# Performance work log

Measured on AMD Instinct MI355X. Metric: run time of the kernel, lower is better.

Reference implementation:

```python
import jax, jax.numpy as jnp
import numpy as np

EPS = 1e-05
N_CLUSTERS = 4


def setup_inputs() -> dict:
    key = jax.random.key(0)
    k1, k2, k3, k4, k5, k6 = jax.random.split(key, 6)
    B, C, H, W = 64, 64, 112, 112
    return {
        "x": jax.random.normal(k1, (B, C, H, W), dtype=jnp.float32),
        "running_mean": jax.random.normal(k2, (C,), dtype=jnp.float32),
        "running_var": jax.random.uniform(k3, (C,), dtype=jnp.float32),
        "weight": jax.random.normal(k4, (C,), dtype=jnp.float32),
        "bias": jax.random.normal(k5, (C,), dtype=jnp.float32),
        "labels": jax.random.randint(k6, (B,), 0, N_CLUSTERS, dtype=jnp.int32),
    }


def reference(x, running_mean, running_var, weight, bias, labels):
    B, C, H, W = x.shape
    hw = H * W
    # per-sample partial sums over spatial dims -> [B, C]
    s = jnp.sum(x, axis=(2, 3))
    ss = jnp.sum(x * x, axis=(2, 3))
    # per-cluster reductions over the batch (gather-reduce) -> [G, C]
    S = jax.ops.segment_sum(s, labels, num_segments=N_CLUSTERS)
    SS = jax.ops.segment_sum(ss, labels, num_segments=N_CLUSTERS)
    cnt = jax.ops.segment_sum(jnp.ones((B,), x.dtype), labels, num_segments=N_CLUSTERS)
    N = cnt[:, None] * hw  # elements per (cluster, channel)
    mean_g = S / jnp.maximum(N, 1.0)
    # unbiased variance (ddof=1), matching torch.var_mean(unbiased=True)
    var_g = (SS - N * mean_g * mean_g) / jnp.maximum(N - 1.0, 1.0)
    # blended stats: 0.2 * cluster + 0.8 * running (BN source) stats; scatter back per sample
    mu = 0.2 * mean_g[labels] + 0.8 * running_mean[None, :]      # [B, C]
    var = 0.2 * var_g[labels] + 0.8 * running_var[None, :]       # [B, C]
    x_n = (x - mu[:, :, None, None]) * jax.lax.rsqrt(var + EPS)[:, :, None, None]
    return x_n * weight[None, :, None, None] + bias[None, :, None, None]
```

## Files before the change

kernel.cpp:

```cpp
#include <hip/hip_runtime.h>

#define HW    12544
#define HW4   3136
#define NCH   64
#define NB    64
#define EPSF  1e-5f

typedef float fvec4 __attribute__((ext_vector_type(4)));


__global__ __launch_bounds__(256) void cn_stats_half(const float* __restrict__ x,
                                                     float* __restrict__ ws,
                                                     int c0) {
    int c = (blockIdx.x & 31) + c0;
    int b = blockIdx.x >> 5;
    int p = b * NCH + c;
    const fvec4* xp = (const fvec4*)(x + (size_t)p * HW);
    float s = 0.0f, ss = 0.0f;
    for (int i = threadIdx.x; i < HW4; i += 256) {
        fvec4 v = xp[i];
        s  += v.x + v.y + v.z + v.w;
        ss += v.x * v.x + v.y * v.y + v.z * v.z + v.w * v.w;
    }
    #pragma unroll
    for (int off = 32; off > 0; off >>= 1) {
        s  += __shfl_down(s, off, 64);
        ss += __shfl_down(ss, off, 64);
    }
    __shared__ float sh[8];
    int lane = threadIdx.x & 63;
    int wave = threadIdx.x >> 6;
    if (lane == 0) { sh[wave] = s; sh[4 + wave] = ss; }
    __syncthreads();
    if (threadIdx.x == 0) {
        ws[p]        = sh[0] + sh[1] + sh[2] + sh[3];
        ws[4096 + p] = sh[4] + sh[5] + sh[6] + sh[7];
    }
}

__global__ __launch_bounds__(256) void cn_norm_half(const float* __restrict__ x,
                                                    const int* __restrict__ labels,
                                                    const float* __restrict__ rmean,
                                                    const float* __restrict__ rvar,
                                                    const float* __restrict__ wgt,
                                                    const float* __restrict__ bia,
                                                    const float* __restrict__ ws,
                                                    float* __restrict__ out,
                                                    int c0) {
    int c = (blockIdx.x & 31) + c0;
    int b = blockIdx.x >> 5;
    int p = b * NCH + c;
    __shared__ float sh_scale, sh_shift;
    if (threadIdx.x < 64) {
        int t = threadIdx.x;
        int g  = labels[b];
        int lb = labels[t];
        bool m = (lb == g);
        float s   = m ? ws[t * NCH + c]        : 0.0f;
        float ss  = m ? ws[4096 + t * NCH + c] : 0.0f;
        float cnt = m ? 1.0f : 0.0f;
        #pragma unroll
        for (int off = 32; off > 0; off >>= 1) {
            s   += __shfl_down(s,   off, 64);
            ss  += __shfl_down(ss,  off, 64);
            cnt += __shfl_down(cnt, off, 64);
        }
        if (t == 0) {
            float N    = cnt * (float)HW;
            float mean = s / fmaxf(N, 1.0f);
            float var  = (ss - N * mean * mean) / fmaxf(N - 1.0f, 1.0f);
            float mu   = 0.2f * mean + 0.8f * rmean[c];
            float vb   = 0.2f * var  + 0.8f * rvar[c];
            float scale = rsqrtf(vb + EPSF) * wgt[c];
            sh_scale = scale;
            sh_shift = bia[c] - mu * scale;
        }
    }
    __syncthreads();
    float scale = sh_scale;
    float shift = sh_shift;
    const fvec4* xp = (const fvec4*)(x + (size_t)p * HW);
    fvec4*       op = (fvec4*)(out + (size_t)p * HW);
    for (int i = threadIdx.x; i < HW4; i += 256) {
        fvec4 v = __builtin_nontemporal_load(&xp[i]);
        fvec4 o;
        o.x = v.x * scale + shift;
        o.y = v.y * scale + shift;
        o.z = v.z * scale + shift;
        o.w = v.w * scale + shift;
        __builtin_nontemporal_store(o, &op[i]);
    }
}

extern "C" void kernel_launch(void* const* d_in, const int* in_sizes, int n_in,
                              void* d_out, int out_size, void* d_ws, size_t ws_size,
                              hipStream_t stream) {
    const float* x      = (const float*)d_in[0];
    const float* rmean  = (const float*)d_in[1];
    const float* rvar   = (const float*)d_in[2];
    const float* wgt    = (const float*)d_in[3];
    const float* bia    = (const float*)d_in[4];
    const int*   labels = (const int*)d_in[5];
    float* out = (float*)d_out;
    float* ws  = (float*)d_ws;

    const int half = NB * (NCH / 2);

    cn_stats_half<<<half, 256, 0, stream>>>(x, ws, 0);
    cn_norm_half <<<half, 256, 0, stream>>>(x, labels, rmean, rvar, wgt, bia, ws, out, 0);
    cn_stats_half<<<half, 256, 0, stream>>>(x, ws, 32);
    cn_norm_half <<<half, 256, 0, stream>>>(x, labels, rmean, rvar, wgt, bia, ws, out, 32);
}
```

Baseline: 101.2 us.

## Pipeline channel-chunk stats with normalization of the previous chunk in one launch

Replaces the two-half stats/normalize sequence with nine launches over 8-channel chunks. Each launch computes statistics for chunk k while normalizing chunk k-1, so the second read of x hits a much smaller, more cache-resident working set and the two phases overlap. The normalize path also switches from a nontemporal load to a regular load so it can reuse the cached data. The cost is more kernel launches and a boundary between launches for each chunk.

```diff
diff --git a/kernel.cpp b/kernel.cpp
--- a/kernel.cpp
+++ b/kernel.cpp
@@ -9,86 +9,87 @@
 typedef float fvec4 __attribute__((ext_vector_type(4)));
 
 
-__global__ __launch_bounds__(256) void cn_stats_half(const float* __restrict__ x,
-                                                     float* __restrict__ ws,
-                                                     int c0) {
-    int c = (blockIdx.x & 31) + c0;
-    int b = blockIdx.x >> 5;
-    int p = b * NCH + c;
-    const fvec4* xp = (const fvec4*)(x + (size_t)p * HW);
-    float s = 0.0f, ss = 0.0f;
-    for (int i = threadIdx.x; i < HW4; i += 256) {
-        fvec4 v = xp[i];
-        s  += v.x + v.y + v.z + v.w;
-        ss += v.x * v.x + v.y * v.y + v.z * v.z + v.w * v.w;
-    }
-    #pragma unroll
-    for (int off = 32; off > 0; off >>= 1) {
-        s  += __shfl_down(s, off, 64);
-        ss += __shfl_down(ss, off, 64);
-    }
-    __shared__ float sh[8];
-    int lane = threadIdx.x & 63;
-    int wave = threadIdx.x >> 6;
-    if (lane == 0) { sh[wave] = s; sh[4 + wave] = ss; }
-    __syncthreads();
-    if (threadIdx.x == 0) {
-        ws[p]        = sh[0] + sh[1] + sh[2] + sh[3];
-        ws[4096 + p] = sh[4] + sh[5] + sh[6] + sh[7];
-    }
-}
+__global__ __launch_bounds__(256) void cn_pipe(const float* __restrict__ x,
+                                               const int* __restrict__ labels,
+                                               const float* __restrict__ rmean,
+                                               const float* __restrict__ rvar,
+                                               const float* __restrict__ wgt,
+                                               const float* __restrict__ bia,
+                                               float* __restrict__ ws,
+                                               float* __restrict__ out,
+                                               int c_stats0, int c_norm0) {
+    int half = blockIdx.x >> 9;
+    int idx  = blockIdx.x & 511;
+    int cc   = idx & 7;
+    int b    = idx >> 3;
 
-__global__ __launch_bounds__(256) void cn_norm_half(const float* __restrict__ x,
-                                                    const int* __restrict__ labels,
-                                                    const float* __restrict__ rmean,
-                                                    const float* __restrict__ rvar,
-                                                    const float* __restrict__ wgt,
-                                                    const float* __restrict__ bia,
-                                                    const float* __restrict__ ws,
-                                                    float* __restrict__ out,
-                                                    int c0) {
-    int c = (blockIdx.x & 31) + c0;
-    int b = blockIdx.x >> 5;
-    int p = b * NCH + c;
-    __shared__ float sh_scale, sh_shift;
-    if (threadIdx.x < 64) {
-        int t = threadIdx.x;
-        int g  = labels[b];
-        int lb = labels[t];
-        bool m = (lb == g);
-        float s   = m ? ws[t * NCH + c]        : 0.0f;
-        float ss  = m ? ws[4096 + t * NCH + c] : 0.0f;
-        float cnt = m ? 1.0f : 0.0f;
+    if (half == 1 || c_norm0 < 0) {
+        int c = c_stats0 + cc;
+        int p = b * NCH + c;
+        const fvec4* xp = (const fvec4*)(x + (size_t)p * HW);
+        float s = 0.0f, ss = 0.0f;
+        for (int i = threadIdx.x; i < HW4; i += 256) {
+            fvec4 v = xp[i];
+            s  += v.x + v.y + v.z + v.w;
+            ss += v.x * v.x + v.y * v.y + v.z * v.z + v.w * v.w;
+        }
         #pragma unroll
         for (int off = 32; off > 0; off >>= 1) {
-            s   += __shfl_down(s,   off, 64);
-            ss  += __shfl_down(ss,  off, 64);
-            cnt += __shfl_down(cnt, off, 64);
+            s  += __shfl_down(s, off, 64);
+            ss += __shfl_down(ss, off, 64);
         }
-        if (t == 0) {
-            float N    = cnt * (float)HW;
-            float mean = s / fmaxf(N, 1.0f);
-            float var  = (ss - N * mean * mean) / fmaxf(N - 1.0f, 1.0f);
-            float mu   = 0.2f * mean + 0.8f * rmean[c];
-            float vb   = 0.2f * var  + 0.8f * rvar[c];
-            float scale = rsqrtf(vb + EPSF) * wgt[c];
-            sh_scale = scale;
-            sh_shift = bia[c] - mu * scale;
+        __shared__ float sh[8];
+        int lane = threadIdx.x & 63;
+        int wave = threadIdx.x >> 6;
+        if (lane == 0) { sh[wave] = s; sh[4 + wave] = ss; }
+        __syncthreads();
+        if (threadIdx.x == 0) {
+            ws[p]        = sh[0] + sh[1] + sh[2] + sh[3];
+            ws[4096 + p] = sh[4] + sh[5] + sh[6] + sh[7];
         }
-    }
-    __syncthreads();
-    float scale = sh_scale;
-    float shift = sh_shift;
-    const fvec4* xp = (const fvec4*)(x + (size_t)p * HW);
-    fvec4*       op = (fvec4*)(out + (size_t)p * HW);
-    for (int i = threadIdx.x; i < HW4; i += 256) {
-        fvec4 v = __builtin_nontemporal_load(&xp[i]);
-        fvec4 o;
-        o.x = v.x * scale + shift;
-        o.y = v.y * scale + shift;
-        o.z = v.z * scale + shift;
-        o.w = v.w * scale + shift;
-        __builtin_nontemporal_store(o, &op[i]);
+    } else {
+        int c = c_norm0 + cc;
+        int p = b * NCH + c;
+        __shared__ float sh_scale, sh_shift;
+        if (threadIdx.x < 64) {
+            int t  = threadIdx.x;
+            int g  = labels[b];
+            int lb = labels[t];
+            bool m = (lb == g);
+            float s   = m ? ws[t * NCH + c]        : 0.0f;
+            float ss  = m ? ws[4096 + t * NCH + c] : 0.0f;
+            float cnt = m ? 1.0f : 0.0f;
+            #pragma unroll
+            for (int off = 32; off > 0; off >>= 1) {
+                s   += __shfl_down(s,   off, 64);
+                ss  += __shfl_down(ss,  off, 64);
+                cnt += __shfl_down(cnt, off, 64);
+            }
+            if (t == 0) {
+                float N    = cnt * (float)HW;
+                float mean = s / fmaxf(N, 1.0f);
+                float var  = (ss - N * mean * mean) / fmaxf(N - 1.0f, 1.0f);
+                float mu   = 0.2f * mean + 0.8f * rmean[c];
+                float vb   = 0.2f * var  + 0.8f * rvar[c];
+                float scale = rsqrtf(vb + EPSF) * wgt[c];
+                sh_scale = scale;
+                sh_shift = bia[c] - mu * scale;
+            }
+        }
+        __syncthreads();
+        float scale = sh_scale;
+        float shift = sh_shift;
+        const fvec4* xp = (const fvec4*)(x + (size_t)p * HW);
+        fvec4*       op = (fvec4*)(out + (size_t)p * HW);
+        for (int i = threadIdx.x; i < HW4; i += 256) {
+            fvec4 v = xp[i];
+            fvec4 o;
+            o.x = v.x * scale + shift;
+            o.y = v.y * scale + shift;
+            o.z = v.z * scale + shift;
+            o.w = v.w * scale + shift;
+            __builtin_nontemporal_store(o, &op[i]);
+        }
     }
 }
 
@@ -104,10 +105,10 @@
     float* out = (float*)d_out;
     float* ws  = (float*)d_ws;
 
-    const int half = NB * (NCH / 2);
-
-    cn_stats_half<<<half, 256, 0, stream>>>(x, ws, 0);
-    cn_norm_half <<<half, 256, 0, stream>>>(x, labels, rmean, rvar, wgt, bia, ws, out, 0);
-    cn_stats_half<<<half, 256, 0, stream>>>(x, ws, 32);
-    cn_norm_half <<<half, 256, 0, stream>>>(x, labels, rmean, rvar, wgt, bia, ws, out, 32);
+    cn_pipe<<<512, 256, 0, stream>>>(x, labels, rmean, rvar, wgt, bia, ws, out, 0, -1);
+    for (int k = 1; k < 8; ++k) {
+        cn_pipe<<<1024, 256, 0, stream>>>(x, labels, rmean, rvar, wgt, bia, ws, out,
+                                          8 * k, 8 * (k - 1));
+    }
+    cn_pipe<<<512, 256, 0, stream>>>(x, labels, rmean, rvar, wgt, bia, ws, out, 0, 56);
 }
```

Measured after the change: 106.5 us. 1.05x slower.
